# Optimization experiments

Measured on AMD Instinct MI355X. Metric: run time of the kernel, lower is better.

## Reference

```python
import jax, jax.numpy as jnp
import numpy as np

EPS = 1e-5

def layer_norm(x, g, b):
    m = x.mean(-1, keepdims=True)
    v = ((x - m) ** 2).mean(-1, keepdims=True)
    return (x - m) / jnp.sqrt(v + EPS) * g + b

def lstm(x_sbd, W_ih, W_hh, b_ih, b_hh):
    # x_sbd: (S, B, D); PyTorch gate order i, f, g, o
    S, B, D = x_sbd.shape
    H = W_hh.shape[1]
    h0 = jnp.zeros((B, H), x_sbd.dtype)
    c0 = jnp.zeros((B, H), x_sbd.dtype)
    def step(carry, x_t):
        h, c = carry
        gates = x_t @ W_ih.T + b_ih + h @ W_hh.T + b_hh
        i, f, g, o = jnp.split(gates, 4, axis=-1)
        c = jax.nn.sigmoid(f) * c + jax.nn.sigmoid(i) * jnp.tanh(g)
        h = jax.nn.sigmoid(o) * jnp.tanh(c)
        return (h, c), h
    (hL, _), hs = jax.lax.scan(step, (h0, c0), x_sbd)
    return hs, hL  # (S,B,H), (B,H)

def setup_inputs():
    key = jax.random.key(0)
    ks = jax.random.split(key, 20)
    B, S, D, V = 64, 1024, 128, 50000
    sc = 1.0 / np.sqrt(D)
    r = lambda k, shp, s=sc: (jax.random.normal(k, shp, jnp.float32) * s)
    return {
        "new_list": jax.random.randint(ks[0], (B, S), 0, V, jnp.int32),
        "new_mask": jnp.ones((B, S), jnp.float32),
        "aspect": jax.random.randint(ks[1], (B, 1), 0, V, jnp.int32),
        "gpunum": 0,
        "emb": r(ks[2], (V, D), 0.02),
        "W_ih": r(ks[3], (4 * D, D)),
        "W_hh": r(ks[4], (4 * D, D)),
        "b_ih": jnp.zeros((4 * D,), jnp.float32),
        "b_hh": jnp.zeros((4 * D,), jnp.float32),
        "an_g": jnp.ones((D,), jnp.float32),
        "an_b": jnp.zeros((D,), jnp.float32),
        "hn_g": jnp.ones((D,), jnp.float32),
        "hn_b": jnp.zeros((D,), jnp.float32),
        "W_att": r(ks[5], (D, D)),
        "W_aw": r(ks[6], (1, D)),
        "W_rout": r(ks[7], (D, D)),
        "W_hout": r(ks[8], (D, D)),
        "W_cls": r(ks[9], (2, D)),
        "b_cls": jnp.zeros((2,), jnp.float32),
    }

def reference(new_list, new_mask, aspect, gpunum, emb, W_ih, W_hh, b_ih, b_hh,
              an_g, an_b, hn_g, hn_b, W_att, W_aw, W_rout, W_hout, W_cls, b_cls):
    # embed, seq-major for LSTM
    x = emb[new_list.T]                      # (S, B, D)
    hidden_output, h_L = lstm(x, W_ih, W_hh, b_ih, b_hh)
    aspect_emb = emb[aspect]                 # (B, 1, D)
    aspect_emb = layer_norm(aspect_emb, an_g, an_b)
    hidden_output = layer_norm(hidden_output, hn_g, hn_b)
    hid = jnp.transpose(hidden_output, (1, 0, 2))  # (B, S, D)
    # circular convolution along hidden dim via FFT (batched; replaces host scipy loop)
    M = jnp.real(jnp.fft.ifft(jnp.fft.fft(hid, axis=-1) * jnp.fft.fft(aspect_emb, axis=-1), axis=-1)).astype(hid.dtype)
    # self-attention: key=M, value=hid, mask applied before softmax (as in original)
    QK = jnp.tanh(M @ W_att.T)               # (B, S, D)
    QK = new_mask[..., None] * QK
    weight = jax.nn.softmax(QK @ W_aw.T, axis=1)  # (B, S, 1)
    r = jnp.einsum('bs,bsd->bd', weight[..., 0], hid)
    r = jnp.tanh(r @ W_rout.T + h_L @ W_hout.T)
    result = jax.nn.softmax(r @ W_cls.T + b_cls, axis=-1)
    return (result, r)
```

## Files before the change

kernel.cpp:

```cpp
#include <hip/hip_runtime.h>

typedef __attribute__((ext_vector_type(8))) short s16x8;
typedef __attribute__((ext_vector_type(4))) float f32x4;
typedef __attribute__((ext_vector_type(4))) unsigned short u16x4;
typedef __attribute__((ext_vector_type(8))) unsigned short u16x8;

#define PAD 136
#define LPAD 144
#define SSTR (4*LPAD+8)

__device__ __forceinline__ unsigned short f2bf(float f){
  union{float f;unsigned u;} v; v.f=f;
  unsigned r=v.u + 0x7fffu + ((v.u>>16)&1u);
  return (unsigned short)(r>>16);
}
__device__ __forceinline__ float bf2f(unsigned short u){
  union{unsigned u;float f;} v; v.u=((unsigned)u)<<16; return v.f;
}
__device__ __forceinline__ float ubits2f(unsigned u){
  union{unsigned u;float f;} v; v.u=u; return v.f;
}
__device__ __forceinline__ float rcp_(float x){ return __builtin_amdgcn_rcpf(x); }
__device__ __forceinline__ float e2_(float x){ return __builtin_amdgcn_exp2f(x); }
__device__ __forceinline__ float tanh_(float x){ return 1.f-2.f*rcp_(1.f+e2_(x*2.885390082f)); }

__device__ __forceinline__ void mfma128(const unsigned short* As, const unsigned short* Bs, f32x4 acc[4][2]){
  const int tid=threadIdx.x, w=tid>>6, l=tid&63;
  const int wm=w>>2, wn=w&3, lr=l&15, lk=(l>>4)*8;
#pragma unroll
  for(int kc=0;kc<4;++kc){
    const int ko=kc*32+lk;
    s16x8 a[4], bb[2];
#pragma unroll
    for(int mt=0;mt<4;++mt) a[mt]=*(const s16x8*)(As+(wm*64+mt*16+lr)*PAD+ko);
#pragma unroll
    for(int nt=0;nt<2;++nt) bb[nt]=*(const s16x8*)(Bs+(wn*32+nt*16+lr)*PAD+ko);
#pragma unroll
    for(int mt=0;mt<4;++mt)
#pragma unroll
      for(int nt=0;nt<2;++nt)
        acc[mt][nt]=__builtin_amdgcn_mfma_f32_16x16x32_bf16(a[mt],bb[nt],acc[mt][nt],0,0,0);
  }
}

__global__ __launch_bounds__(256) void k_cvt(const float* __restrict__ w, unsigned short* __restrict__ o, int n){
  int i = blockIdx.x*256 + threadIdx.x;
  if (i<n){
    int g=(i>>14)&3;
    float s=(g==2)?-2.885390082f:-1.442695041f;
    o[i] = f2bf(w[i]*s);
  }
}

__global__ __launch_bounds__(512) void k_aspg(const int* __restrict__ aspect, const float* __restrict__ emb,
    const float* __restrict__ ang, const float* __restrict__ anb, const float* __restrict__ watt,
    unsigned short* __restrict__ gt){
  __shared__ unsigned short As[128*PAD];
  __shared__ unsigned short Bs[128*PAD];
  __shared__ float a_ln[128];
  __shared__ float stat[2];
  const int b=blockIdx.x, tid=threadIdx.x;
  if (tid<128) a_ln[tid] = emb[(size_t)aspect[b]*128 + tid];
  __syncthreads();
  if (tid==0){
    float s=0.f,q=0.f;
    for(int d=0;d<128;++d){ float v=a_ln[d]; s+=v; q+=v*v; }
    float m=s*(1.f/128.f);
    stat[0]=m; stat[1]=__builtin_amdgcn_rsqf(q*(1.f/128.f)-m*m+1e-5f);
  }
  __syncthreads();
  if (tid<128) a_ln[tid] = (a_ln[tid]-stat[0])*stat[1]*ang[tid]+anb[tid];
  __syncthreads();
  {
    int k=tid>>2, dq=(tid&3)*32;
    for(int d=dq; d<dq+32; ++d) As[k*PAD+d]=f2bf(a_ln[(d-k)&127]);
  }
  {
    int i=tid>>2, kq=(tid&3)*32;
    const f32x4* src=(const f32x4*)(watt+(size_t)i*128+kq);
#pragma unroll
    for(int j=0;j<8;++j){ f32x4 v=src[j]; u16x4 o;
#pragma unroll
      for(int q=0;q<4;++q) o[q]=f2bf(v[q]);
      *(u16x4*)(Bs+i*PAD+kq+4*j)=o; }
  }
  __syncthreads();
  f32x4 z={0.f,0.f,0.f,0.f};
  f32x4 acc[4][2]={{z,z},{z,z},{z,z},{z,z}};
  mfma128(As,Bs,acc);
  const int w=tid>>6,l=tid&63,wm=w>>2,wn=w&3,lr=l&15,lg=l>>4;
#pragma unroll
  for(int mt=0;mt<4;++mt)
#pragma unroll
    for(int nt=0;nt<2;++nt){
      int k0=wm*64+mt*16+lg*4;
      int n=wn*32+nt*16+lr;
      u16x4 o;
#pragma unroll
      for(int r=0;r<4;++r) o[r]=f2bf(acc[mt][nt][r]);
      *(u16x4*)(gt+(size_t)b*16384+n*128+k0)=o;
    }
}

__global__ __launch_bounds__(512) void k_xw(const int* __restrict__ new_list, const float* __restrict__ emb,
    const float* __restrict__ wih, const float* __restrict__ bih, const float* __restrict__ bhh,
    unsigned short* __restrict__ xw){
  __shared__ unsigned short As[128*PAD];
  __shared__ unsigned short Bs[128*PAD];
  const int tid=threadIdx.x;
  const int m0=blockIdx.x*128, n0=blockIdx.y*128;
  {
    int i=tid>>2, kq=(tid&3)*32;
    int m=m0+i, t=m>>6, b=m&63;
    int tok=new_list[b*1024+t];
    const f32x4* src=(const f32x4*)(emb+(size_t)tok*128+kq);
#pragma unroll
    for(int j=0;j<8;++j){ f32x4 v=src[j]; u16x4 o;
#pragma unroll
      for(int q=0;q<4;++q) o[q]=f2bf(v[q]);
      *(u16x4*)(As+i*PAD+kq+4*j)=o; }
  }
  {
    int i=tid>>2, kq=(tid&3)*32;
    const f32x4* src=(const f32x4*)(wih+(size_t)(n0+i)*128+kq);
#pragma unroll
    for(int j=0;j<8;++j){ f32x4 v=src[j]; u16x4 o;
#pragma unroll
      for(int q=0;q<4;++q) o[q]=f2bf(v[q]);
      *(u16x4*)(Bs+i*PAD+kq+4*j)=o; }
  }
  __syncthreads();
  f32x4 z={0.f,0.f,0.f,0.f};
  f32x4 acc[4][2]={{z,z},{z,z},{z,z},{z,z}};
  mfma128(As,Bs,acc);
  const int w=tid>>6,l=tid&63,wm=w>>2,wn=w&3,lr=l&15,lg=l>>4;
#pragma unroll
  for(int nt=0;nt<2;++nt){
    int n=n0+wn*32+nt*16+lr;
    float bias=bih[n]+bhh[n];
    float s=((n>>7)==2)?-2.885390082f:-1.442695041f;
#pragma unroll
    for(int mt=0;mt<4;++mt){
      int m_=m0+wm*64+mt*16+lg*4;
      int t=m_>>6, b0=m_&63;
      u16x4 o;
#pragma unroll
      for(int r=0;r<4;++r) o[r]=f2bf((acc[mt][nt][r]+bias)*s);
      *(u16x4*)(xw+(((size_t)t*16+(b0>>2))*512+n)*4)=o;
    }
  }
}

__global__ __launch_bounds__(512) void k_lstm(const unsigned short* __restrict__ xw,
    const unsigned short* __restrict__ whh,
    unsigned short* __restrict__ hraw, float* __restrict__ hL){
  __shared__ unsigned short hbuf[8][SSTR];
  const int tid=threadIdx.x, w=tid>>6, l=tid&63, lr=l&15, lg=l>>4;
  const int blk=blockIdx.x, bb=blk*4;
  const int cb=w*16+lr;
  s16x8 wf[4][4];
#pragma unroll
  for(int g=0;g<4;++g)
#pragma unroll
    for(int kc=0;kc<4;++kc)
      wf[g][kc]=*(const s16x8*)(whh+(size_t)(g*128+cb)*128+kc*32+lg*8);
  for(int i=tid;i<8*SSTR;i+=512) ((unsigned short*)hbuf)[i]=0;
  __syncthreads();
  const unsigned short* x0 = xw + (size_t)blk*2048;
  int xofs[4];
#pragma unroll
  for(int g=0;g<4;++g) xofs[g]=((g*128+cb)<<2)+lg;
  unsigned short px[4], p1[4];
#pragma unroll
  for(int g=0;g<4;++g) px[g]=x0[xofs[g]];
#pragma unroll
  for(int g=0;g<4;++g) p1[g]=x0[32768+xofs[g]];
  const int ro=tid>>7, ss=(tid>>4)&7, c0=(tid&15)*8;
  const unsigned short* hls=&hbuf[ss][ro*LPAD+c0];
  unsigned short* hst = hraw + ((size_t)(bb+ro)<<17) + (ss<<7) + c0;
  float cc=0.f, hh=0.f;
  for(int t=0;t<1024;++t){
    if ((t&7)==0 && t){
      u16x8 v=*(const u16x8*)hls;
      *(u16x8*)(hst + ((size_t)(t-8)<<7)) = v;
      asm volatile("s_waitcnt lgkmcnt(0)\n\ts_barrier" ::: "memory");
    }
    const unsigned short* hc=hbuf[(t+7)&7];
    s16x8 af[4];
#pragma unroll
    for(int kc=0;kc<4;++kc) af[kc]=*(const s16x8*)(hc+(lr>>2)*LPAD+kc*32+lg*8);
    int t2=t+2<1024?t+2:1023;
    const unsigned short* xq=x0+(size_t)t2*32768;
    unsigned short pn[4];
#pragma unroll
    for(int g=0;g<4;++g) pn[g]=xq[xofs[g]];
    f32x4 z={0.f,0.f,0.f,0.f};
    f32x4 acc[4]={z,z,z,z};
#pragma unroll
    for(int kc=0;kc<4;++kc)
#pragma unroll
      for(int g=0;g<4;++g)
        acc[g]=__builtin_amdgcn_mfma_f32_16x16x32_bf16(af[kc],wf[g][kc],acc[g],0,0,0);
    float ex[4];
#pragma unroll
    for(int g=0;g<4;++g){
      float a=acc[g][0]+ubits2f(((unsigned)px[g])<<16);
      if (g==2) a=__builtin_amdgcn_fmed3f(a,-80.f,80.f);
      ex[g]=e2_(a);
      px[g]=p1[g]; p1[g]=pn[g];
    }
    float sitg=rcp_((1.f+ex[0])*(1.f+ex[2]))*(1.f-ex[2]);
    float sf=rcp_(1.f+ex[1]);
    cc=fmaf(sf,cc,sitg);
    float cl=__builtin_amdgcn_fmed3f(cc,-30.f,30.f);
    float E=e2_(cl*2.885390082f);
    hh=(E-1.f)*rcp_((1.f+ex[3])*(E+1.f));
    unsigned p;
    asm("v_cvt_pk_bf16_f32 %0, %1, %2":"=v"(p):"v"(hh),"v"(hh));
    hbuf[t&7][lg*LPAD+cb]=(unsigned short)(p&0xffffu);
    asm volatile("s_waitcnt lgkmcnt(0)\n\ts_barrier" ::: "memory");
  }
  {
    u16x8 v=*(const u16x8*)hls;
    *(u16x8*)(hst + ((size_t)1016<<7)) = v;
  }
  hL[(size_t)(bb+lg)*128+cb]=hh;
}

__global__ __launch_bounds__(512) void k_scores(const unsigned short* __restrict__ hraw,
    const unsigned short* __restrict__ gt, const float* __restrict__ hng, const float* __restrict__ hnb,
    const float* __restrict__ waw, const float* __restrict__ mask,
    unsigned short* __restrict__ hln, float* __restrict__ scores){
  __shared__ unsigned short As[128*PAD];
  __shared__ unsigned short Bs[128*PAD];
  __shared__ float redS[128][4];
  __shared__ float redQ[128][4];
  __shared__ float red[128][4];
  const int b=blockIdx.x>>3, s0=(blockIdx.x&7)*128;
  const int tid=threadIdx.x;
  const int i=tid>>2, kq=(tid&3)*32;
  u16x8 hv[4];
  {
    const u16x8* src=(const u16x8*)(hraw+((size_t)b*1024+s0+i)*128+kq);
    float s=0.f,q=0.f;
#pragma unroll
    for(int j=0;j<4;++j){ hv[j]=src[j];
#pragma unroll
      for(int e=0;e<8;++e){ float x=bf2f(hv[j][e]); s+=x; q+=x*x; } }
    redS[i][tid&3]=s; redQ[i][tid&3]=q;
  }
  {
    const u16x4* src=(const u16x4*)(gt+(size_t)b*16384+i*128+kq);
#pragma unroll
    for(int j=0;j<8;++j) *(u16x4*)(Bs+i*PAD+kq+4*j)=src[j];
  }
  __syncthreads();
  {
    float s=redS[i][0]+redS[i][1]+redS[i][2]+redS[i][3];
    float q=redQ[i][0]+redQ[i][1]+redQ[i][2]+redQ[i][3];
    float m=s*(1.f/128.f);
    float inv=__builtin_amdgcn_rsqf(q*(1.f/128.f)-m*m+1e-5f);
    unsigned short* dst=hln+((size_t)b*1024+s0+i)*128+kq;
#pragma unroll
    for(int j=0;j<4;++j){ u16x8 o;
#pragma unroll
      for(int e=0;e<8;++e){ int d=kq+j*8+e;
        float x=(bf2f(hv[j][e])-m)*inv*hng[d]+hnb[d];
        o[e]=f2bf(x); }
      *(u16x8*)(As+i*PAD+kq+8*j)=o;
      *(u16x8*)(dst+8*j)=o;
    }
  }
  __syncthreads();
  f32x4 z={0.f,0.f,0.f,0.f};
  f32x4 acc[4][2]={{z,z},{z,z},{z,z},{z,z}};
  mfma128(As,Bs,acc);
  const int w=tid>>6,l=tid&63,wm=w>>2,wn=w&3,lr=l&15,lg=l>>4;
  const float w0=waw[wn*32+lr], w1=waw[wn*32+16+lr];
#pragma unroll
  for(int mt=0;mt<4;++mt){
    f32x4 p4;
#pragma unroll
    for(int r=0;r<4;++r) p4[r]=tanh_(acc[mt][0][r])*w0+tanh_(acc[mt][1][r])*w1;
#pragma unroll
    for(int m=1;m<16;m<<=1){
#pragma unroll
      for(int r=0;r<4;++r) p4[r]+=__shfl_xor(p4[r],m,64);
    }
    if (lr==0){
#pragma unroll
      for(int r=0;r<4;++r) red[wm*64+mt*16+lg*4+r][wn]=p4[r];
    }
  }
  __syncthreads();
  if (tid<128){
    float sc=red[tid][0]+red[tid][1]+red[tid][2]+red[tid][3];
    sc*=mask[b*1024+s0+tid];
    scores[b*1024+s0+tid]=sc;
  }
}

__global__ __launch_bounds__(256) void k_wsum(const float* __restrict__ scores,
    const unsigned short* __restrict__ hln, float* __restrict__ rpre){
  __shared__ float wl[1024];
  __shared__ float red[256];
  __shared__ float part[8][32];
  const int b=blockIdx.x>>2, d0=(blockIdx.x&3)*32;
  const int tid=threadIdx.x;
  float v[4]; float lm=-1e30f;
#pragma unroll
  for(int q=0;q<4;++q){ v[q]=scores[b*1024+tid+256*q]; lm=fmaxf(lm,v[q]); }
  red[tid]=lm; __syncthreads();
  for(int st=128;st;st>>=1){ if(tid<st) red[tid]=fmaxf(red[tid],red[tid+st]); __syncthreads(); }
  const float mx=red[0]; __syncthreads();
  float ls=0.f;
#pragma unroll
  for(int q=0;q<4;++q){ v[q]=e2_((v[q]-mx)*1.442695041f); ls+=v[q]; }
  red[tid]=ls; __syncthreads();
  for(int st=128;st;st>>=1){ if(tid<st) red[tid]+=red[tid+st]; __syncthreads(); }
  const float inv=rcp_(red[0]);
#pragma unroll
  for(int q=0;q<4;++q) wl[tid+256*q]=v[q]*inv;
  __syncthreads();
  const int d=tid&31, sg=tid>>5;
  float acc=0.f;
  const unsigned short* hp=hln+(size_t)b*131072+d0+d;
  for(int s=sg*128;s<sg*128+128;++s) acc+=wl[s]*bf2f(hp[(size_t)s*128]);
  part[sg][d]=acc; __syncthreads();
  if (tid<32){
    float a=0.f;
#pragma unroll
    for(int g=0;g<8;++g) a+=part[g][tid];
    rpre[b*128+d0+tid]=a;
  }
}

__global__ __launch_bounds__(128) void k_final(const float* __restrict__ rpre, const float* __restrict__ hLp,
    const float* __restrict__ wrout, const float* __restrict__ whout, const float* __restrict__ wcls,
    const float* __restrict__ bcls, float* __restrict__ out){
  __shared__ float rv[128], hv[128], cred[4];
  const int b=blockIdx.x, n=threadIdx.x;
  rv[n]=rpre[b*128+n]; hv[n]=hLp[b*128+n];
  __syncthreads();
  float a=0.f;
  const float* wr=wrout+(size_t)n*128;
  const float* wh=whout+(size_t)n*128;
  for(int k=0;k<128;++k) a+=rv[k]*wr[k]+hv[k]*wh[k];
  const float rr=tanh_(a);
  out[128+b*128+n]=rr;
  float p0=rr*wcls[n], p1=rr*wcls[128+n];
#pragma unroll
  for(int m=1;m<64;m<<=1){ p0+=__shfl_xor(p0,m,64); p1+=__shfl_xor(p1,m,64); }
  if ((n&63)==0){ cred[(n>>6)*2]=p0; cred[(n>>6)*2+1]=p1; }
  __syncthreads();
  if (n==0){
    float l0=cred[0]+cred[2]+bcls[0], l1=cred[1]+cred[3]+bcls[1];
    float m=fmaxf(l0,l1);
    float e0=e2_((l0-m)*1.442695041f), e1=e2_((l1-m)*1.442695041f);
    float s=rcp_(e0+e1);
    out[b*2]=e0*s; out[b*2+1]=e1*s;
  }
}

extern "C" void kernel_launch(void* const* d_in, const int* in_sizes, int n_in,
                              void* d_out, int out_size, void* d_ws, size_t ws_size,
                              hipStream_t stream) {
  (void)in_sizes; (void)n_in; (void)out_size; (void)ws_size;
  const int*   new_list=(const int*)d_in[0];
  const float* new_mask=(const float*)d_in[1];
  const int*   aspect  =(const int*)d_in[2];
  const float* emb   =(const float*)d_in[4];
  const float* W_ih  =(const float*)d_in[5];
  const float* W_hh  =(const float*)d_in[6];
  const float* b_ih  =(const float*)d_in[7];
  const float* b_hh  =(const float*)d_in[8];
  const float* an_g  =(const float*)d_in[9];
  const float* an_b  =(const float*)d_in[10];
  const float* hn_g  =(const float*)d_in[11];
  const float* hn_b  =(const float*)d_in[12];
  const float* W_att =(const float*)d_in[13];
  const float* W_aw  =(const float*)d_in[14];
  const float* W_rout=(const float*)d_in[15];
  const float* W_hout=(const float*)d_in[16];
  const float* W_cls =(const float*)d_in[17];
  const float* b_cls =(const float*)d_in[18];
  float* out=(float*)d_out;
  char* ws=(char*)d_ws;
  unsigned short* xw    =(unsigned short*)(ws);
  unsigned short* hraw  =(unsigned short*)(ws+67108864);
  unsigned short* hln   =(unsigned short*)(ws+83886080);
  unsigned short* gt    =(unsigned short*)(ws+100663296);
  unsigned short* whh   =(unsigned short*)(ws+102760448);
  float*          scores=(float*)(ws+102891520);
  float*          hLb   =(float*)(ws+103153664);
  float*          rpre  =(float*)(ws+103186432);
  k_cvt   <<<dim3(256),    dim3(256), 0, stream>>>(W_hh, whh, 512*128);
  k_aspg  <<<dim3(64),     dim3(512), 0, stream>>>(aspect, emb, an_g, an_b, W_att, gt);
  k_xw    <<<dim3(512,4),  dim3(512), 0, stream>>>(new_list, emb, W_ih, b_ih, b_hh, xw);
  k_lstm  <<<dim3(16),     dim3(512), 0, stream>>>(xw, whh, hraw, hLb);
  k_scores<<<dim3(512),    dim3(512), 0, stream>>>(hraw, gt, hn_g, hn_b, W_aw, new_mask, hln, scores);
  k_wsum  <<<dim3(256),    dim3(256), 0, stream>>>(scores, hln, rpre);
  k_final <<<dim3(64),     dim3(128), 0, stream>>>(rpre, hLb, W_rout, W_hout, W_cls, b_cls, out);
}
```

Measured before the change: 603.9 us.

## Double-buffer LSTM hidden state and store each step directly to global

The 8-slot shared ring buffer with batched 16-byte flushes every 8 steps becomes a 2-slot ping-pong buffer, and each thread writes its bf16 hidden value straight to global memory every step. The extra barrier every 8 steps goes away. The MFMA chain is split into two independent accumulators to shorten the dependency chain, and the precomputed input projections are converted to float one step earlier. The trade is narrow 2-byte scattered global stores issued on every step of the serial recurrence.

```diff
diff --git a/kernel.cpp b/kernel.cpp
--- a/kernel.cpp
+++ b/kernel.cpp
@@ -7,7 +7,6 @@
 
 #define PAD 136
 #define LPAD 144
-#define SSTR (4*LPAD+8)
 
 __device__ __forceinline__ unsigned short f2bf(float f){
   union{float f;unsigned u;} v; v.f=f;
@@ -154,7 +153,7 @@
 __global__ __launch_bounds__(512) void k_lstm(const unsigned short* __restrict__ xw,
     const unsigned short* __restrict__ whh,
     unsigned short* __restrict__ hraw, float* __restrict__ hL){
-  __shared__ unsigned short hbuf[8][SSTR];
+  __shared__ unsigned short hbuf[2][4*LPAD];
   const int tid=threadIdx.x, w=tid>>6, l=tid&63, lr=l&15, lg=l>>4;
   const int blk=blockIdx.x, bb=blk*4;
   const int cb=w*16+lr;
@@ -164,50 +163,47 @@
 #pragma unroll
     for(int kc=0;kc<4;++kc)
       wf[g][kc]=*(const s16x8*)(whh+(size_t)(g*128+cb)*128+kc*32+lg*8);
-  for(int i=tid;i<8*SSTR;i+=512) ((unsigned short*)hbuf)[i]=0;
+  for(int i=tid;i<2*4*LPAD;i+=512) ((unsigned short*)hbuf)[i]=0;
   __syncthreads();
   const unsigned short* x0 = xw + (size_t)blk*2048;
   int xofs[4];
 #pragma unroll
   for(int g=0;g<4;++g) xofs[g]=((g*128+cb)<<2)+lg;
-  unsigned short px[4], p1[4];
-#pragma unroll
-  for(int g=0;g<4;++g) px[g]=x0[xofs[g]];
-#pragma unroll
-  for(int g=0;g<4;++g) p1[g]=x0[32768+xofs[g]];
-  const int ro=tid>>7, ss=(tid>>4)&7, c0=(tid&15)*8;
-  const unsigned short* hls=&hbuf[ss][ro*LPAD+c0];
-  unsigned short* hst = hraw + ((size_t)(bb+ro)<<17) + (ss<<7) + c0;
+  float pxf[4], p1f[4];
+#pragma unroll
+  for(int g=0;g<4;++g) pxf[g]=ubits2f(((unsigned)x0[xofs[g]])<<16);
+#pragma unroll
+  for(int g=0;g<4;++g) p1f[g]=ubits2f(((unsigned)x0[32768+xofs[g]])<<16);
+  unsigned short* hrp=hraw+((size_t)(bb+lg)<<17)+cb;
   float cc=0.f, hh=0.f;
+  int cur=0;
   for(int t=0;t<1024;++t){
-    if ((t&7)==0 && t){
-      u16x8 v=*(const u16x8*)hls;
-      *(u16x8*)(hst + ((size_t)(t-8)<<7)) = v;
-      asm volatile("s_waitcnt lgkmcnt(0)\n\ts_barrier" ::: "memory");
-    }
-    const unsigned short* hc=hbuf[(t+7)&7];
-    s16x8 af[4];
-#pragma unroll
-    for(int kc=0;kc<4;++kc) af[kc]=*(const s16x8*)(hc+(lr>>2)*LPAD+kc*32+lg*8);
+    const unsigned short* hc=hbuf[cur];
+    s16x8 af0=*(const s16x8*)(hc+(lr>>2)*LPAD+ 0+lg*8);
+    s16x8 af1=*(const s16x8*)(hc+(lr>>2)*LPAD+32+lg*8);
+    s16x8 af2=*(const s16x8*)(hc+(lr>>2)*LPAD+64+lg*8);
+    s16x8 af3=*(const s16x8*)(hc+(lr>>2)*LPAD+96+lg*8);
     int t2=t+2<1024?t+2:1023;
     const unsigned short* xq=x0+(size_t)t2*32768;
-    unsigned short pn[4];
-#pragma unroll
-    for(int g=0;g<4;++g) pn[g]=xq[xofs[g]];
+    float pnf[4];
+#pragma unroll
+    for(int g=0;g<4;++g) pnf[g]=ubits2f(((unsigned)xq[xofs[g]])<<16);
     f32x4 z={0.f,0.f,0.f,0.f};
-    f32x4 acc[4]={z,z,z,z};
-#pragma unroll
-    for(int kc=0;kc<4;++kc)
-#pragma unroll
-      for(int g=0;g<4;++g)
-        acc[g]=__builtin_amdgcn_mfma_f32_16x16x32_bf16(af[kc],wf[g][kc],acc[g],0,0,0);
+    f32x4 aA[4]={z,z,z,z}, aB[4]={z,z,z,z};
+#pragma unroll
+    for(int g=0;g<4;++g){
+      aA[g]=__builtin_amdgcn_mfma_f32_16x16x32_bf16(af0,wf[g][0],aA[g],0,0,0);
+      aB[g]=__builtin_amdgcn_mfma_f32_16x16x32_bf16(af2,wf[g][2],aB[g],0,0,0);
+      aA[g]=__builtin_amdgcn_mfma_f32_16x16x32_bf16(af1,wf[g][1],aA[g],0,0,0);
+      aB[g]=__builtin_amdgcn_mfma_f32_16x16x32_bf16(af3,wf[g][3],aB[g],0,0,0);
+    }
     float ex[4];
 #pragma unroll
     for(int g=0;g<4;++g){
-      float a=acc[g][0]+ubits2f(((unsigned)px[g])<<16);
+      float a=aA[g][0]+aB[g][0]+pxf[g];
       if (g==2) a=__builtin_amdgcn_fmed3f(a,-80.f,80.f);
       ex[g]=e2_(a);
-      px[g]=p1[g]; p1[g]=pn[g];
+      pxf[g]=p1f[g]; p1f[g]=pnf[g];
     }
     float sitg=rcp_((1.f+ex[0])*(1.f+ex[2]))*(1.f-ex[2]);
     float sf=rcp_(1.f+ex[1]);
@@ -217,12 +213,11 @@
     hh=(E-1.f)*rcp_((1.f+ex[3])*(E+1.f));
     unsigned p;
     asm("v_cvt_pk_bf16_f32 %0, %1, %2":"=v"(p):"v"(hh),"v"(hh));
-    hbuf[t&7][lg*LPAD+cb]=(unsigned short)(p&0xffffu);
+    unsigned short hb=(unsigned short)(p&0xffffu);
+    hbuf[cur^1][lg*LPAD+cb]=hb;
+    hrp[(size_t)t<<7]=hb;
     asm volatile("s_waitcnt lgkmcnt(0)\n\ts_barrier" ::: "memory");
-  }
-  {
-    u16x8 v=*(const u16x8*)hls;
-    *(u16x8*)(hst + ((size_t)1016<<7)) = v;
+    cur^=1;
   }
   hL[(size_t)(bb+lg)*128+cb]=hh;
 }
```

After: 618.6 us. +2.4%, slower.
